# Kernel optimization log

Measured on AMD Instinct MI355X. Metric: run time of the kernel, lower is better.

The kernel has to match this reference:

```python
import jax, jax.numpy as jnp
import numpy as np

N_ENT = 50000
N_REL = 200
N_EDGE = 1_000_000
D = 64


def setup_inputs() -> dict:
    key = jax.random.key(0)
    ks = jax.random.split(key, 12)
    src = jax.random.randint(ks[0], (N_EDGE,), 0, N_ENT)
    rel = jax.random.randint(ks[1], (N_EDGE,), 0, N_REL)
    dst = jax.random.randint(ks[2], (N_EDGE,), 0, N_ENT)
    triples = jnp.stack([src, rel, dst], axis=1).astype(jnp.int64)  # [E,3]
    s = 1.0 / np.sqrt(D)
    return {
        "emb_e": jax.random.normal(ks[3], (N_ENT, D), jnp.float32) * s,
        "re_att": jax.random.normal(ks[4], (N_REL,), jnp.float32) * 0.1,
        "W1": jax.random.normal(ks[5], (D, D), jnp.float32) * s,
        "W2": jax.random.normal(ks[6], (D, D), jnp.float32) * s,
        "W3": jax.random.normal(ks[7], (D, D), jnp.float32) * s,
        "u": jax.random.normal(ks[8], (3 * D,), jnp.float32) * s,
        "en_weight": jax.random.normal(ks[9], (D, D), jnp.float32) * s,
        "re_weight": jax.random.normal(ks[10], (D, D), jnp.float32) * s,
        "re_spec": jax.random.normal(ks[11], (D,), jnp.float32) * s,
        "triples": triples,
    }


def _forward(emb_e, re_att, W1, W2, W3, u, en_weight, re_weight, re_spec, triples):
    src = triples[:, 0]
    rel = triples[:, 1]
    dst = triples[:, 2]
    n = emb_e.shape[0]

    def wgc(x, W):
        # relation-weighted message passing: out[s] += w[r] * x[d]
        msg = jax.ops.segment_sum(x[dst] * re_att[rel][:, None], src, num_segments=n)
        return jnp.tanh((x + msg) @ W)

    x = wgc(emb_e, W1)
    x = wgc(x, W2)
    x = wgc(x, W3)

    # GAT-style edge scores: e = LeakyReLU(u . [W_en h_i ; W_re r_spec ; W_en h_j])
    d = x.shape[1]
    hs = x @ en_weight.T                       # [N,d] = (en_weight @ h)^T rows
    z_src = hs @ u[:d]                         # [N]
    z_dst = hs @ u[2 * d:]                     # [N]
    z_mid = u[d:2 * d] @ (re_weight @ re_spec)  # scalar, same for every edge
    scores = jax.nn.leaky_relu(z_src[src] + z_mid + z_dst[dst], 0.01)  # [E]

    # softmax normalized over ALL triples (global denominator, per source code)
    alpha = jax.nn.softmax(scores)

    # out[src] += alpha_e * x[dst]
    out = jax.ops.segment_sum(alpha[:, None] * x[dst], src, num_segments=n)
    return out


def reference(emb_e, re_att, W1, W2, W3, u, en_weight, re_weight, re_spec, triples):
    return _forward(emb_e, re_att, W1, W2, W3, u, en_weight, re_weight, re_spec, triples)
```

## Files before the change

kernel.cpp:

```cpp
#include <hip/hip_runtime.h>
#include <math.h>

#define N_ENT  50000
#define N_REL  200
#define N_EDGE 1000000
#define CHUNK  196
#define NCH    64
#define ECH2   15625
#define NPART  8
#define NRNG   6250

#define WS_MISC   0
#define WS_ZSUM   128
#define WS_ZMID   192
#define WS_AV     256
#define WS_BV     512
#define WS_BSUM   0x00010000
#define WS_BBASE  0x00011000
#define WS_TOT    0x00040000
#define WS_OFFS   0x00080000
#define WS_ZSRC   0x000C0000
#define WS_ZDST   0x00100000
#define WS_SNODE  0x00140000
#define WS_SRCS   0x00180000
#define WS_EB     0x00380000
#define WS_EPK    0x00780000
#define WS_HIST   0x00B80000
#define WS_XB1    0x00B80000
#define WS_XB0    0x01200000

__device__ __forceinline__ float bflo(unsigned u) { return __uint_as_float(u << 16); }
__device__ __forceinline__ float bfhi(unsigned u) { return __uint_as_float(u & 0xffff0000u); }
__device__ __forceinline__ unsigned short f2bf(float f) {
  unsigned u = __float_as_uint(f);
  unsigned r = ((u >> 16) & 1u) + 0x7fffu;
  return (unsigned short)((u + r) >> 16);
}
__device__ __forceinline__ float lanebc(float v, int k) {
  return __uint_as_float((unsigned)__builtin_amdgcn_readlane((int)__float_as_uint(v), k));
}
__device__ __forceinline__ float fast_tanh(float x) {
  float ex = __expf(2.f * x);
  return 1.f - __fdividef(2.f, ex + 1.f);
}
__device__ __forceinline__ void fma8(float* acc, float wt, uint4 q) {
  acc[0] += wt * bflo(q.x); acc[1] += wt * bfhi(q.x);
  acc[2] += wt * bflo(q.y); acc[3] += wt * bfhi(q.y);
  acc[4] += wt * bflo(q.z); acc[5] += wt * bfhi(q.z);
  acc[6] += wt * bflo(q.w); acc[7] += wt * bfhi(q.w);
}

__global__ void k_init(const void* tri, int* misc, double* zsum) {
  if (blockIdx.x == 0 && threadIdx.x < 64) {
    int l = threadIdx.x;
    int z = ((const int*)tri)[2 * l + 1];
    unsigned long long m = __ballot(z == 0);
    if (l == 0) { misc[0] = (m == ~0ull) ? 1 : 0; *zsum = 0.0; }
  }
}

__global__ void k_conv(const float* __restrict__ x, unsigned short* __restrict__ xb) {
  int i = blockIdx.x * blockDim.x + threadIdx.x;
  if (i >= N_ENT * 16) return;
  float4 v = ((const float4*)x)[i];
  ushort4 o;
  o.x = f2bf(v.x); o.y = f2bf(v.y); o.z = f2bf(v.z); o.w = f2bf(v.w);
  ((ushort4*)xb)[i] = o;
}

__global__ void k_decode(const void* tri, unsigned short* __restrict__ srcs,
                         unsigned* __restrict__ eb, const int* misc) {
  int is64 = misc[0];
  int stride = gridDim.x * blockDim.x;
  if (is64) {
    const long long* t = (const long long*)tri;
    for (int e = blockIdx.x * blockDim.x + threadIdx.x; e < N_EDGE; e += stride) {
      int s = (int)t[3 * e], r = (int)t[3 * e + 1], d = (int)t[3 * e + 2];
      srcs[e] = (unsigned short)s;
      eb[e] = ((unsigned)r << 16) | (unsigned)d;
    }
  } else {
    const int* t = (const int*)tri;
    for (int e = blockIdx.x * blockDim.x + threadIdx.x; e < N_EDGE; e += stride) {
      int s = t[3 * e], r = t[3 * e + 1], d = t[3 * e + 2];
      srcs[e] = (unsigned short)s;
      eb[e] = ((unsigned)r << 16) | (unsigned)d;
    }
  }
}

__global__ void __launch_bounds__(256) k_hist(const unsigned short* __restrict__ srcs,
                                              unsigned short* __restrict__ hist) {
  __shared__ unsigned h[NRNG];
  int c = blockIdx.x >> 3, x = blockIdx.x & 7;
  int lo = x * NRNG;
  for (int i = threadIdx.x; i < NRNG; i += 256) h[i] = 0u;
  __syncthreads();
  int e0 = c * ECH2, e1 = e0 + ECH2;
  for (int e = e0 + threadIdx.x; e < e1; e += 256) {
    int rel = (int)srcs[e] - lo;
    if ((unsigned)rel < NRNG) atomicAdd(&h[rel], 1u);
  }
  __syncthreads();
  for (int i = threadIdx.x; i < NRNG; i += 256)
    hist[c * N_ENT + lo + i] = (unsigned short)h[i];
}

__global__ void k_scanH(unsigned short* __restrict__ hist, int* __restrict__ tot) {
  int s = blockIdx.x * blockDim.x + threadIdx.x;
  if (s >= N_ENT) return;
  int run = 0;
  for (int c = 0; c < NCH; c++) {
    int v = hist[c * N_ENT + s];
    hist[c * N_ENT + s] = (unsigned short)run;
    run += v;
  }
  tot[s] = run;
}

__global__ void k_scanA(const int* __restrict__ counts, int* __restrict__ bsum) {
  __shared__ int sm[4];
  int t = threadIdx.x;
  int i = blockIdx.x * CHUNK + t;
  int v = (t < CHUNK && i < N_ENT) ? counts[i] : 0;
  for (int o = 32; o; o >>= 1) v += __shfl_down(v, o);
  if ((t & 63) == 0) sm[t >> 6] = v;
  __syncthreads();
  if (t == 0) bsum[blockIdx.x] = sm[0] + sm[1] + sm[2] + sm[3];
}

__global__ void k_scanB(const int* __restrict__ bsum, int* __restrict__ bbase, int* __restrict__ offs) {
  __shared__ int sm[256];
  int t = threadIdx.x;
  int v = bsum[t];
  sm[t] = v;
  __syncthreads();
  for (int d = 1; d < 256; d <<= 1) {
    int x = (t >= d) ? sm[t - d] : 0;
    __syncthreads();
    sm[t] += x;
    __syncthreads();
  }
  bbase[t] = sm[t] - v;
  if (t == 255) offs[N_ENT] = sm[255];
}

__global__ void k_scanC(const int* __restrict__ counts, const int* __restrict__ bbase,
                        int* __restrict__ offs) {
  __shared__ int sm[256];
  int t = threadIdx.x;
  int i = blockIdx.x * CHUNK + t;
  int v = (t < CHUNK && i < N_ENT) ? counts[i] : 0;
  sm[t] = v;
  __syncthreads();
  for (int d = 1; d < 256; d <<= 1) {
    int x = (t >= d) ? sm[t - d] : 0;
    __syncthreads();
    sm[t] += x;
    __syncthreads();
  }
  if (t < CHUNK && i < N_ENT)
    offs[i] = bbase[blockIdx.x] + sm[t] - v;
}

__global__ void __launch_bounds__(256) k_scatter(
    const unsigned short* __restrict__ srcs, const unsigned* __restrict__ eb,
    const unsigned short* __restrict__ cbase, const int* __restrict__ offs,
    unsigned* __restrict__ epk) {
  __shared__ unsigned h[NRNG];
  int c = blockIdx.x >> 3, x = blockIdx.x & 7;
  int lo = x * NRNG;
  for (int i = threadIdx.x; i < NRNG; i += 256) h[i] = 0u;
  __syncthreads();
  int e0 = c * ECH2, e1 = e0 + ECH2;
  for (int e = e0 + threadIdx.x; e < e1; e += 256) {
    int s = (int)srcs[e];
    int rel = s - lo;
    if ((unsigned)rel < NRNG) {
      int lr = atomicAdd(&h[rel], 1u);
      epk[offs[s] + (int)cbase[c * N_ENT + s] + lr] = eb[e];
    }
  }
}

__global__ void k_pre(const float* u, const float* enw, const float* rew, const float* rsp,
                      float* a, float* b, float* zmid) {
  int k = threadIdx.x;
  float aa = 0.f, bb = 0.f;
  for (int j = 0; j < 64; j++) {
    float w = enw[j * 64 + k];
    aa += u[j] * w;
    bb += u[128 + j] * w;
  }
  a[k] = aa; b[k] = bb;
  float t = 0.f;
  for (int c = 0; c < 64; c++) t += rew[k * 64 + c] * rsp[c];
  t *= u[64 + k];
  for (int o = 32; o; o >>= 1) t += __shfl_down(t, o);
  if (k == 0) *zmid = t;
}

template <int EPI>
__global__ void __launch_bounds__(256) k_wgc(
    const unsigned short* __restrict__ xb, const float* __restrict__ W,
    const int* __restrict__ offs, const unsigned* __restrict__ epk,
    const float* __restrict__ re_att, unsigned short* __restrict__ yb,
    const float* __restrict__ a, const float* __restrict__ b,
    float* __restrict__ zsrc, float* __restrict__ zdst) {
  __shared__ float s_att[N_REL];
  for (int t = threadIdx.x; t < N_REL; t += 256) s_att[t] = re_att[t];
  __syncthreads();
  int wid = (blockIdx.x * blockDim.x + threadIdx.x) >> 6;
  int lane = threadIdx.x & 63;
  if (wid >= N_ENT) return;
  int node = wid;
  int g = lane >> 3, c8 = (lane & 7) * 8;
  int e0 = offs[node], e1 = offs[node + 1];
  float acc[8] = {0.f, 0.f, 0.f, 0.f, 0.f, 0.f, 0.f, 0.f};
  {
    uint4 q = *(const uint4*)(xb + (size_t)node * 64 + c8);
    fma8(acc, (g == 0) ? 1.f : 0.f, q);
  }
  for (int e = e0; e < e1; e += 16) {
    int ia = e + g, ib = ia + 8;
    bool va = ia < e1, vb = ib < e1;
    unsigned pa = epk[va ? ia : e0];
    unsigned pb = epk[vb ? ib : e0];
    float wa = va ? s_att[pa >> 16] : 0.f;
    float wb = vb ? s_att[pb >> 16] : 0.f;
    unsigned ra = va ? (pa & 0xffffu) : 0u;
    unsigned rb = vb ? (pb & 0xffffu) : 0u;
    uint4 qa = *(const uint4*)(xb + (size_t)ra * 64 + c8);
    uint4 qb = *(const uint4*)(xb + (size_t)rb * 64 + c8);
    fma8(acc, wa, qa);
    fma8(acc, wb, qb);
  }
#pragma unroll
  for (int off = 8; off <= 32; off <<= 1)
#pragma unroll
    for (int c = 0; c < 8; c++) acc[c] += __shfl_xor(acc[c], off);
  float o = 0.f;
#pragma unroll
  for (int j = 0; j < 8; j++)
#pragma unroll
    for (int c = 0; c < 8; c++)
      o += lanebc(acc[c], j) * W[(j * 8 + c) * 64 + lane];
  float yv = fast_tanh(o);
  yb[(size_t)node * 64 + lane] = f2bf(yv);
  if (EPI) {
    float za = yv * a[lane], zb = yv * b[lane];
    for (int s = 32; s; s >>= 1) { za += __shfl_down(za, s); zb += __shfl_down(zb, s); }
    if (lane == 0) { zsrc[node] = za; zdst[node] = zb; }
  }
}

__global__ void __launch_bounds__(256) k_out(
    const unsigned short* __restrict__ xb, const int* __restrict__ offs,
    const unsigned* __restrict__ epk, const float* __restrict__ zs,
    const float* __restrict__ zd, const float* zmid,
    float* __restrict__ out, float* __restrict__ snode) {
  int wid = (blockIdx.x * blockDim.x + threadIdx.x) >> 6;
  int lane = threadIdx.x & 63;
  if (wid >= N_ENT) return;
  int node = wid;
  int g = lane >> 3, c8 = (lane & 7) * 8;
  float zi = zs[node] + *zmid;
  float acc[8] = {0.f, 0.f, 0.f, 0.f, 0.f, 0.f, 0.f, 0.f};
  float s0 = 0.f;
  int e0 = offs[node], e1 = offs[node + 1];
  for (int e = e0; e < e1; e += 16) {
    int ia = e + g, ib = ia + 8;
    bool va = ia < e1, vb = ib < e1;
    unsigned pa = epk[va ? ia : e0];
    unsigned pb = epk[vb ? ib : e0];
    unsigned da = va ? (pa & 0xffffu) : 0u;
    unsigned db = vb ? (pb & 0xffffu) : 0u;
    float ca = zi + zd[da];
    float cb = zi + zd[db];
    ca = ca >= 0.f ? ca : 0.01f * ca;
    cb = cb >= 0.f ? cb : 0.01f * cb;
    float wa = va ? __expf(ca) : 0.f;
    float wb = vb ? __expf(cb) : 0.f;
    uint4 qa = *(const uint4*)(xb + (size_t)da * 64 + c8);
    uint4 qb = *(const uint4*)(xb + (size_t)db * 64 + c8);
    fma8(acc, wa, qa);
    fma8(acc, wb, qb);
    s0 += wa + wb;
  }
#pragma unroll
  for (int off = 8; off <= 32; off <<= 1) {
#pragma unroll
    for (int c = 0; c < 8; c++) acc[c] += __shfl_xor(acc[c], off);
    s0 += __shfl_xor(s0, off);
  }
  if (lane < 8) {
    float4* p = (float4*)(out + (size_t)node * 64 + lane * 8);
    p[0] = make_float4(acc[0], acc[1], acc[2], acc[3]);
    p[1] = make_float4(acc[4], acc[5], acc[6], acc[7]);
  }
  if (lane == 0) snode[node] = s0;
}

__global__ void k_red(const float* __restrict__ snode, double* zsum) {
  int stride = gridDim.x * blockDim.x;
  double s = 0.0;
  for (int i = blockIdx.x * blockDim.x + threadIdx.x; i < N_ENT; i += stride)
    s += (double)snode[i];
  for (int o = 32; o; o >>= 1) s += __shfl_down(s, o);
  __shared__ double ws_[4];
  if ((threadIdx.x & 63) == 0) ws_[threadIdx.x >> 6] = s;
  __syncthreads();
  if (threadIdx.x == 0)
    atomicAdd(zsum, ws_[0] + ws_[1] + ws_[2] + ws_[3]);
}

__global__ void k_norm(float* __restrict__ out, const double* zsum) {
  int i = blockIdx.x * blockDim.x + threadIdx.x;
  if (i >= N_ENT * 16) return;
  float invZ = (float)(1.0 / *zsum);
  float4 v = ((float4*)out)[i];
  v.x *= invZ; v.y *= invZ; v.z *= invZ; v.w *= invZ;
  ((float4*)out)[i] = v;
}

extern "C" void kernel_launch(void* const* d_in, const int* in_sizes, int n_in,
                              void* d_out, int out_size, void* d_ws, size_t ws_size,
                              hipStream_t stream) {
  const float* emb   = (const float*)d_in[0];
  const float* reatt = (const float*)d_in[1];
  const float* W1    = (const float*)d_in[2];
  const float* W2    = (const float*)d_in[3];
  const float* W3    = (const float*)d_in[4];
  const float* u     = (const float*)d_in[5];
  const float* enw   = (const float*)d_in[6];
  const float* rew   = (const float*)d_in[7];
  const float* rsp   = (const float*)d_in[8];
  const void*  tri   = d_in[9];

  char* ws = (char*)d_ws;
  int*            misc   = (int*)(ws + WS_MISC);
  double*         zsum   = (double*)(ws + WS_ZSUM);
  float*          zmid   = (float*)(ws + WS_ZMID);
  float*          av     = (float*)(ws + WS_AV);
  float*          bv     = (float*)(ws + WS_BV);
  int*            bsum   = (int*)(ws + WS_BSUM);
  int*            bbase  = (int*)(ws + WS_BBASE);
  int*            tot    = (int*)(ws + WS_TOT);
  int*            offs   = (int*)(ws + WS_OFFS);
  float*          zsrc   = (float*)(ws + WS_ZSRC);
  float*          zdst   = (float*)(ws + WS_ZDST);
  float*          snode  = (float*)(ws + WS_SNODE);
  unsigned short* srcs   = (unsigned short*)(ws + WS_SRCS);
  unsigned*       eb     = (unsigned*)(ws + WS_EB);
  unsigned*       epk    = (unsigned*)(ws + WS_EPK);
  unsigned short* hist   = (unsigned short*)(ws + WS_HIST);
  unsigned short* xb0    = (unsigned short*)(ws + WS_XB0);
  unsigned short* xb1    = (unsigned short*)(ws + WS_XB1);
  float*          out    = (float*)d_out;

  k_init<<<1, 64, 0, stream>>>(tri, misc, zsum);
  k_conv<<<3125, 256, 0, stream>>>(emb, xb0);
  k_decode<<<4096, 256, 0, stream>>>(tri, srcs, eb, misc);
  k_hist<<<NCH * NPART, 256, 0, stream>>>(srcs, hist);
  k_scanH<<<196, 256, 0, stream>>>(hist, tot);
  k_scanA<<<256, 256, 0, stream>>>(tot, bsum);
  k_scanB<<<1, 256, 0, stream>>>(bsum, bbase, offs);
  k_scanC<<<256, 256, 0, stream>>>(tot, bbase, offs);
  k_scatter<<<NCH * NPART, 256, 0, stream>>>(srcs, eb, hist, offs, epk);
  k_pre<<<1, 64, 0, stream>>>(u, enw, rew, rsp, av, bv, zmid);

  int nb = (N_ENT * 64 + 255) / 256;
  k_wgc<0><<<nb, 256, 0, stream>>>(xb0, W1, offs, epk, reatt, xb1, nullptr, nullptr, nullptr, nullptr);
  k_wgc<0><<<nb, 256, 0, stream>>>(xb1, W2, offs, epk, reatt, xb0, nullptr, nullptr, nullptr, nullptr);
  k_wgc<1><<<nb, 256, 0, stream>>>(xb0, W3, offs, epk, reatt, xb1, av, bv, zsrc, zdst);

  k_out<<<nb, 256, 0, stream>>>(xb1, offs, epk, zsrc, zdst, zmid, out, snode);
  k_red<<<196, 256, 0, stream>>>(snode, zsum);
  k_norm<<<3125, 256, 0, stream>>>(out, zsum);
}
```

Before: 250.1 us.

## Use MFMA for WGC dense transform and fuse small setup kernels

Each k_wgc block now handles 16 nodes: wavefronts aggregate 4 nodes each into a shared bf16 tile, and one MFMA 16x16x32 bf16 pair per wavefront multiplies it by a pre-transposed bf16 weight tile, replacing the per-lane readlane dot product. Weight conversion, k_pre, and zsum init are folded into the single-block scan kernel. The int64 detection moves into k_decode, scanA is merged into scanH, and the histogram partition count is halved so each block covers a larger LDS range. The aggregated message and the weights are rounded to bf16 before the matmul, which adds rounding error, and each block now carries extra LDS and barriers.

```diff
diff --git a/kernel.cpp b/kernel.cpp
--- a/kernel.cpp
+++ b/kernel.cpp
@@ -7,14 +7,14 @@
 #define CHUNK  196
 #define NCH    64
 #define ECH2   15625
-#define NPART  8
-#define NRNG   6250
-
-#define WS_MISC   0
+#define NPART  4
+#define NRNG   12500
+
 #define WS_ZSUM   128
 #define WS_ZMID   192
 #define WS_AV     256
 #define WS_BV     512
+#define WS_WT     0x00001000
 #define WS_BSUM   0x00010000
 #define WS_BBASE  0x00011000
 #define WS_TOT    0x00040000
@@ -29,15 +29,18 @@
 #define WS_XB1    0x00B80000
 #define WS_XB0    0x01200000
 
+typedef __attribute__((ext_vector_type(8))) short s16x8;
+typedef __attribute__((ext_vector_type(4))) float f32x4;
+
 __device__ __forceinline__ float bflo(unsigned u) { return __uint_as_float(u << 16); }
 __device__ __forceinline__ float bfhi(unsigned u) { return __uint_as_float(u & 0xffff0000u); }
+__device__ __forceinline__ float bf2f(unsigned short u) {
+  return __uint_as_float(((unsigned)u) << 16);
+}
 __device__ __forceinline__ unsigned short f2bf(float f) {
   unsigned u = __float_as_uint(f);
   unsigned r = ((u >> 16) & 1u) + 0x7fffu;
   return (unsigned short)((u + r) >> 16);
-}
-__device__ __forceinline__ float lanebc(float v, int k) {
-  return __uint_as_float((unsigned)__builtin_amdgcn_readlane((int)__float_as_uint(v), k));
 }
 __device__ __forceinline__ float fast_tanh(float x) {
   float ex = __expf(2.f * x);
@@ -49,14 +52,9 @@
   acc[4] += wt * bflo(q.z); acc[5] += wt * bfhi(q.z);
   acc[6] += wt * bflo(q.w); acc[7] += wt * bfhi(q.w);
 }
-
-__global__ void k_init(const void* tri, int* misc, double* zsum) {
-  if (blockIdx.x == 0 && threadIdx.x < 64) {
-    int l = threadIdx.x;
-    int z = ((const int*)tri)[2 * l + 1];
-    unsigned long long m = __ballot(z == 0);
-    if (l == 0) { misc[0] = (m == ~0ull) ? 1 : 0; *zsum = 0.0; }
-  }
+__device__ __forceinline__ int tri_is64(const void* tri) {
+  int z = ((const int*)tri)[2 * (threadIdx.x & 63) + 1];
+  return __ballot(z == 0) == ~0ull;
 }
 
 __global__ void k_conv(const float* __restrict__ x, unsigned short* __restrict__ xb) {
@@ -69,8 +67,8 @@
 }
 
 __global__ void k_decode(const void* tri, unsigned short* __restrict__ srcs,
-                         unsigned* __restrict__ eb, const int* misc) {
-  int is64 = misc[0];
+                         unsigned* __restrict__ eb) {
+  int is64 = tri_is64(tri);
   int stride = gridDim.x * blockDim.x;
   if (is64) {
     const long long* t = (const long long*)tri;
@@ -92,7 +90,7 @@
 __global__ void __launch_bounds__(256) k_hist(const unsigned short* __restrict__ srcs,
                                               unsigned short* __restrict__ hist) {
   __shared__ unsigned h[NRNG];
-  int c = blockIdx.x >> 3, x = blockIdx.x & 7;
+  int c = blockIdx.x >> 2, x = blockIdx.x & 3;
   int lo = x * NRNG;
   for (int i = threadIdx.x; i < NRNG; i += 256) h[i] = 0u;
   __syncthreads();
@@ -106,30 +104,32 @@
     hist[c * N_ENT + lo + i] = (unsigned short)h[i];
 }
 
-__global__ void k_scanH(unsigned short* __restrict__ hist, int* __restrict__ tot) {
-  int s = blockIdx.x * blockDim.x + threadIdx.x;
-  if (s >= N_ENT) return;
+__global__ void __launch_bounds__(256) k_scanH(unsigned short* __restrict__ hist,
+                                               int* __restrict__ tot, int* __restrict__ bsum) {
+  int t = threadIdx.x;
+  int s = blockIdx.x * CHUNK + t;
   int run = 0;
-  for (int c = 0; c < NCH; c++) {
-    int v = hist[c * N_ENT + s];
-    hist[c * N_ENT + s] = (unsigned short)run;
-    run += v;
-  }
-  tot[s] = run;
-}
-
-__global__ void k_scanA(const int* __restrict__ counts, int* __restrict__ bsum) {
+  if (t < CHUNK && s < N_ENT) {
+    for (int c = 0; c < NCH; c++) {
+      int v = hist[c * N_ENT + s];
+      hist[c * N_ENT + s] = (unsigned short)run;
+      run += v;
+    }
+    tot[s] = run;
+  }
+  int v = run;
+  for (int o = 32; o; o >>= 1) v += __shfl_down(v, o);
   __shared__ int sm[4];
-  int t = threadIdx.x;
-  int i = blockIdx.x * CHUNK + t;
-  int v = (t < CHUNK && i < N_ENT) ? counts[i] : 0;
-  for (int o = 32; o; o >>= 1) v += __shfl_down(v, o);
   if ((t & 63) == 0) sm[t >> 6] = v;
   __syncthreads();
   if (t == 0) bsum[blockIdx.x] = sm[0] + sm[1] + sm[2] + sm[3];
 }
 
-__global__ void k_scanB(const int* __restrict__ bsum, int* __restrict__ bbase, int* __restrict__ offs) {
+__global__ void __launch_bounds__(256) k_scanBpre(
+    const int* __restrict__ bsum, int* __restrict__ bbase, int* __restrict__ offs,
+    double* zsum, const float* u, const float* enw, const float* rew, const float* rsp,
+    float* av, float* bv, float* zmid,
+    const float* W1, const float* W2, const float* W3, unsigned short* wt) {
   __shared__ int sm[256];
   int t = threadIdx.x;
   int v = bsum[t];
@@ -143,6 +143,28 @@
   }
   bbase[t] = sm[t] - v;
   if (t == 255) offs[N_ENT] = sm[255];
+  if (t == 0) *zsum = 0.0;
+  if (t < 64) {
+    int k = t;
+    float aa = 0.f, bb = 0.f;
+    for (int j = 0; j < 64; j++) {
+      float w = enw[j * 64 + k];
+      aa += u[j] * w;
+      bb += u[128 + j] * w;
+    }
+    av[k] = aa; bv[k] = bb;
+    float z = 0.f;
+    for (int c = 0; c < 64; c++) z += rew[k * 64 + c] * rsp[c];
+    z *= u[64 + k];
+    for (int o = 32; o; o >>= 1) z += __shfl_down(z, o);
+    if (k == 0) *zmid = z;
+  }
+  for (int idx = t; idx < 4096; idx += 256) {
+    int k = idx >> 6, n = idx & 63;
+    wt[0 * 4608 + n * 72 + k] = f2bf(W1[idx]);
+    wt[1 * 4608 + n * 72 + k] = f2bf(W2[idx]);
+    wt[2 * 4608 + n * 72 + k] = f2bf(W3[idx]);
+  }
 }
 
 __global__ void k_scanC(const int* __restrict__ counts, const int* __restrict__ bbase,
@@ -168,7 +190,7 @@
     const unsigned short* __restrict__ cbase, const int* __restrict__ offs,
     unsigned* __restrict__ epk) {
   __shared__ unsigned h[NRNG];
-  int c = blockIdx.x >> 3, x = blockIdx.x & 7;
+  int c = blockIdx.x >> 2, x = blockIdx.x & 3;
   int lo = x * NRNG;
   for (int i = threadIdx.x; i < NRNG; i += 256) h[i] = 0u;
   __syncthreads();
@@ -183,74 +205,99 @@
   }
 }
 
-__global__ void k_pre(const float* u, const float* enw, const float* rew, const float* rsp,
-                      float* a, float* b, float* zmid) {
-  int k = threadIdx.x;
-  float aa = 0.f, bb = 0.f;
-  for (int j = 0; j < 64; j++) {
-    float w = enw[j * 64 + k];
-    aa += u[j] * w;
-    bb += u[128 + j] * w;
-  }
-  a[k] = aa; b[k] = bb;
-  float t = 0.f;
-  for (int c = 0; c < 64; c++) t += rew[k * 64 + c] * rsp[c];
-  t *= u[64 + k];
-  for (int o = 32; o; o >>= 1) t += __shfl_down(t, o);
-  if (k == 0) *zmid = t;
-}
-
 template <int EPI>
 __global__ void __launch_bounds__(256) k_wgc(
-    const unsigned short* __restrict__ xb, const float* __restrict__ W,
+    const unsigned short* __restrict__ xb, const unsigned short* __restrict__ wt,
     const int* __restrict__ offs, const unsigned* __restrict__ epk,
     const float* __restrict__ re_att, unsigned short* __restrict__ yb,
-    const float* __restrict__ a, const float* __restrict__ b,
+    const float* __restrict__ av, const float* __restrict__ bv,
     float* __restrict__ zsrc, float* __restrict__ zdst) {
+  __shared__ __align__(16) unsigned short s_m[16 * 72];
+  __shared__ __align__(16) unsigned short s_wt[64 * 72];
   __shared__ float s_att[N_REL];
-  for (int t = threadIdx.x; t < N_REL; t += 256) s_att[t] = re_att[t];
-  __syncthreads();
-  int wid = (blockIdx.x * blockDim.x + threadIdx.x) >> 6;
-  int lane = threadIdx.x & 63;
-  if (wid >= N_ENT) return;
-  int node = wid;
+  for (int i = threadIdx.x; i < N_REL; i += 256) s_att[i] = re_att[i];
+  for (int i = threadIdx.x; i < 1152; i += 256)
+    ((uint2*)s_wt)[i] = ((const uint2*)wt)[i];
+  __syncthreads();
+
+  int wv = threadIdx.x >> 6, lane = threadIdx.x & 63;
   int g = lane >> 3, c8 = (lane & 7) * 8;
-  int e0 = offs[node], e1 = offs[node + 1];
-  float acc[8] = {0.f, 0.f, 0.f, 0.f, 0.f, 0.f, 0.f, 0.f};
+  float fa = 0.f, fb = 0.f;
+  if (EPI) { fa = av[lane]; fb = bv[lane]; }
+
+  for (int i = 0; i < 4; i++) {
+    int nl = wv * 4 + i;
+    int node = blockIdx.x * 16 + nl;
+    int e0 = offs[node], e1 = offs[node + 1];
+    float acc[8] = {0.f, 0.f, 0.f, 0.f, 0.f, 0.f, 0.f, 0.f};
+    {
+      uint4 q = *(const uint4*)(xb + (size_t)node * 64 + c8);
+      fma8(acc, (g == 0) ? 1.f : 0.f, q);
+    }
+    for (int e = e0; e < e1; e += 16) {
+      int ia = e + g, ib = ia + 8;
+      bool va = ia < e1, vb = ib < e1;
+      unsigned pa = epk[va ? ia : e0];
+      unsigned pb = epk[vb ? ib : e0];
+      float wa = va ? s_att[pa >> 16] : 0.f;
+      float wb = vb ? s_att[pb >> 16] : 0.f;
+      unsigned ra = va ? (pa & 0xffffu) : 0u;
+      unsigned rb = vb ? (pb & 0xffffu) : 0u;
+      uint4 qa = *(const uint4*)(xb + (size_t)ra * 64 + c8);
+      uint4 qb = *(const uint4*)(xb + (size_t)rb * 64 + c8);
+      fma8(acc, wa, qa);
+      fma8(acc, wb, qb);
+    }
+#pragma unroll
+    for (int off = 8; off <= 32; off <<= 1)
+#pragma unroll
+      for (int c = 0; c < 8; c++) acc[c] += __shfl_xor(acc[c], off);
+    if (lane < 8) {
+      uint4 pk;
+      pk.x = (unsigned)f2bf(acc[0]) | ((unsigned)f2bf(acc[1]) << 16);
+      pk.y = (unsigned)f2bf(acc[2]) | ((unsigned)f2bf(acc[3]) << 16);
+      pk.z = (unsigned)f2bf(acc[4]) | ((unsigned)f2bf(acc[5]) << 16);
+      pk.w = (unsigned)f2bf(acc[6]) | ((unsigned)f2bf(acc[7]) << 16);
+      *(uint4*)&s_m[nl * 72 + lane * 8] = pk;
+    }
+  }
+  __syncthreads();
+
+  int ar = (lane & 15) * 72 + (lane >> 4) * 8;
+  int br = (wv * 16 + (lane & 15)) * 72 + (lane >> 4) * 8;
+  s16x8 a0 = *(const s16x8*)&s_m[ar];
+  s16x8 a1 = *(const s16x8*)&s_m[ar + 32];
+  s16x8 b0 = *(const s16x8*)&s_wt[br];
+  s16x8 b1 = *(const s16x8*)&s_wt[br + 32];
+  f32x4 c = {0.f, 0.f, 0.f, 0.f};
+  c = __builtin_amdgcn_mfma_f32_16x16x32_bf16(a0, b0, c, 0, 0, 0);
+  c = __builtin_amdgcn_mfma_f32_16x16x32_bf16(a1, b1, c, 0, 0, 0);
+  __syncthreads();
+#pragma unroll
+  for (int q = 0; q < 4; q++) {
+    int r = (lane >> 4) * 4 + q;
+    s_m[r * 72 + wv * 16 + (lane & 15)] = f2bf(fast_tanh(c[q]));
+  }
+  __syncthreads();
+
   {
-    uint4 q = *(const uint4*)(xb + (size_t)node * 64 + c8);
-    fma8(acc, (g == 0) ? 1.f : 0.f, q);
-  }
-  for (int e = e0; e < e1; e += 16) {
-    int ia = e + g, ib = ia + 8;
-    bool va = ia < e1, vb = ib < e1;
-    unsigned pa = epk[va ? ia : e0];
-    unsigned pb = epk[vb ? ib : e0];
-    float wa = va ? s_att[pa >> 16] : 0.f;
-    float wb = vb ? s_att[pb >> 16] : 0.f;
-    unsigned ra = va ? (pa & 0xffffu) : 0u;
-    unsigned rb = vb ? (pb & 0xffffu) : 0u;
-    uint4 qa = *(const uint4*)(xb + (size_t)ra * 64 + c8);
-    uint4 qb = *(const uint4*)(xb + (size_t)rb * 64 + c8);
-    fma8(acc, wa, qa);
-    fma8(acc, wb, qb);
-  }
-#pragma unroll
-  for (int off = 8; off <= 32; off <<= 1)
-#pragma unroll
-    for (int c = 0; c < 8; c++) acc[c] += __shfl_xor(acc[c], off);
-  float o = 0.f;
-#pragma unroll
-  for (int j = 0; j < 8; j++)
-#pragma unroll
-    for (int c = 0; c < 8; c++)
-      o += lanebc(acc[c], j) * W[(j * 8 + c) * 64 + lane];
-  float yv = fast_tanh(o);
-  yb[(size_t)node * 64 + lane] = f2bf(yv);
+    int r = threadIdx.x >> 4, c0 = (threadIdx.x & 15) * 4;
+    ushort4 o;
+    o.x = s_m[r * 72 + c0]; o.y = s_m[r * 72 + c0 + 1];
+    o.z = s_m[r * 72 + c0 + 2]; o.w = s_m[r * 72 + c0 + 3];
+    *(ushort4*)(yb + ((size_t)blockIdx.x * 16 + r) * 64 + c0) = o;
+  }
   if (EPI) {
-    float za = yv * a[lane], zb = yv * b[lane];
-    for (int s = 32; s; s >>= 1) { za += __shfl_down(za, s); zb += __shfl_down(zb, s); }
-    if (lane == 0) { zsrc[node] = za; zdst[node] = zb; }
+    for (int i = 0; i < 4; i++) {
+      int nl = wv * 4 + i;
+      float yf = bf2f(s_m[nl * 72 + lane]);
+      float za = yf * fa, zb = yf * fb;
+      for (int s = 32; s; s >>= 1) { za += __shfl_down(za, s); zb += __shfl_down(zb, s); }
+      if (lane == 0) {
+        int node = blockIdx.x * 16 + nl;
+        zsrc[node] = za; zdst[node] = zb;
+      }
+    }
   }
 }
 
@@ -338,11 +385,11 @@
   const void*  tri   = d_in[9];
 
   char* ws = (char*)d_ws;
-  int*            misc   = (int*)(ws + WS_MISC);
   double*         zsum   = (double*)(ws + WS_ZSUM);
   float*          zmid   = (float*)(ws + WS_ZMID);
   float*          av     = (float*)(ws + WS_AV);
   float*          bv     = (float*)(ws + WS_BV);
+  unsigned short* wt     = (unsigned short*)(ws + WS_WT);
   int*            bsum   = (int*)(ws + WS_BSUM);
   int*            bbase  = (int*)(ws + WS_BBASE);
   int*            tot    = (int*)(ws + WS_TOT);
@@ -358,23 +405,23 @@
   unsigned short* xb1    = (unsigned short*)(ws + WS_XB1);
   float*          out    = (float*)d_out;
 
-  k_init<<<1, 64, 0, stream>>>(tri, misc, zsum);
   k_conv<<<3125, 256, 0, stream>>>(emb, xb0);
-  k_decode<<<4096, 256, 0, stream>>>(tri, srcs, eb, misc);
+  k_decode<<<4096, 256, 0, stream>>>(tri, srcs, eb);
   k_hist<<<NCH * NPART, 256, 0, stream>>>(srcs, hist);
-  k_scanH<<<196, 256, 0, stream>>>(hist, tot);
-  k_scanA<<<256, 256, 0, stream>>>(tot, bsum);
-  k_scanB<<<1, 256, 0, stream>>>(bsum, bbase, offs);
+  k_scanH<<<256, 256, 0, stream>>>(hist, tot, bsum);
+  k_scanBpre<<<1, 256, 0, stream>>>(bsum, bbase, offs, zsum, u, enw, rew, rsp,
+                                    av, bv, zmid, W1, W2, W3, wt);
   k_scanC<<<256, 256, 0, stream>>>(tot, bbase, offs);
   k_scatter<<<NCH * NPART, 256, 0, stream>>>(srcs, eb, hist, offs, epk);
-  k_pre<<<1, 64, 0, stream>>>(u, enw, rew, rsp, av, bv, zmid);
-
-  int nb = (N_ENT * 64 + 255) / 256;
-  k_wgc<0><<<nb, 256, 0, stream>>>(xb0, W1, offs, epk, reatt, xb1, nullptr, nullptr, nullptr, nullptr);
-  k_wgc<0><<<nb, 256, 0, stream>>>(xb1, W2, offs, epk, reatt, xb0, nullptr, nullptr, nullptr, nullptr);
-  k_wgc<1><<<nb, 256, 0, stream>>>(xb0, W3, offs, epk, reatt, xb1, av, bv, zsrc, zdst);
-
-  k_out<<<nb, 256, 0, stream>>>(xb1, offs, epk, zsrc, zdst, zmid, out, snode);
+
+  k_wgc<0><<<3125, 256, 0, stream>>>(xb0, wt + 0 * 4608, offs, epk, reatt, xb1,
+                                     nullptr, nullptr, nullptr, nullptr);
+  k_wgc<0><<<3125, 256, 0, stream>>>(xb1, wt + 1 * 4608, offs, epk, reatt, xb0,
+                                     nullptr, nullptr, nullptr, nullptr);
+  k_wgc<1><<<3125, 256, 0, stream>>>(xb0, wt + 2 * 4608, offs, epk, reatt, xb1,
+                                     av, bv, zsrc, zdst);
+
+  k_out<<<12500, 256, 0, stream>>>(xb1, offs, epk, zsrc, zdst, zmid, out, snode);
   k_red<<<196, 256, 0, stream>>>(snode, zsum);
   k_norm<<<3125, 256, 0, stream>>>(out, zsum);
 }
```

After: 224.7 us, median of 2. 10.1% less time.
